# Kernel tuning notes

Measured on AMD Instinct MI355X. Metric: run time of the kernel, lower is better.

The kernel has to match this reference:

```python
import jax, jax.numpy as jnp
import numpy as np

NUM_GROUPS = 32
EPS = 1e-6


def group_norm(x, gamma, beta):
    # x: [b, c, h, w]
    b, c, h, w = x.shape
    xg = x.reshape(b, NUM_GROUPS, c // NUM_GROUPS, h, w)
    mean = xg.mean(axis=(2, 3, 4), keepdims=True)
    var = xg.var(axis=(2, 3, 4), keepdims=True)
    xn = ((xg - mean) * jax.lax.rsqrt(var + EPS)).reshape(b, c, h, w)
    return xn * gamma[None, :, None, None] + beta[None, :, None, None]


def conv1x1(x, w, bias):
    # 1x1 conv == channel-mixing matmul. x: [b,c,h,w], w: [co,ci]
    y = jnp.einsum('bchw,oc->bohw', x, w)
    return y + bias[None, :, None, None]


def setup_inputs() -> dict:
    key = jax.random.key(0)
    ks = jax.random.split(key, 10)
    B, C, H, W = 4, 512, 64, 64
    s = 1.0 / np.sqrt(C)
    inp = {
        'x': jax.random.normal(ks[0], (B, C, H, W), jnp.float32),
        'gamma': jnp.ones((C,), jnp.float32),
        'beta': jnp.zeros((C,), jnp.float32),
        'wq': jax.random.normal(ks[1], (C, C), jnp.float32) * s,
        'bq': jnp.zeros((C,), jnp.float32),
        'wk': jax.random.normal(ks[2], (C, C), jnp.float32) * s,
        'bk': jnp.zeros((C,), jnp.float32),
        'wv': jax.random.normal(ks[3], (C, C), jnp.float32) * s,
        'bv': jnp.zeros((C,), jnp.float32),
        'wo': jax.random.normal(ks[4], (C, C), jnp.float32) * s,
        'bo': jnp.zeros((C,), jnp.float32),
    }
    return inp


def reference(x, gamma, beta, wq, bq, wk, bk, wv, bv, wo, bo):
    b, c, h, w = x.shape
    h_ = group_norm(x, gamma, beta)
    q = conv1x1(h_, wq, bq).reshape(b, c, h * w)  # [b,c,n]
    k = conv1x1(h_, wk, bk).reshape(b, c, h * w)
    v = conv1x1(h_, wv, bv).reshape(b, c, h * w)
    scale = jnp.asarray(c, x.dtype) ** -0.5
    # scores: [b, n, n] = q^T k
    scores = jnp.einsum('bcn,bcm->bnm', q, k) * scale
    attn = jax.nn.softmax(scores, axis=2)
    # out: [b, c, n] = v @ attn^T  (h_[i] = sum_j attn[i,j] v[j])
    out = jnp.einsum('bnm,bcm->bcn', attn, v).reshape(b, c, h, w)
    out = conv1x1(out, wo, bo)
    return x + out
```

## Files before the change

kernel.cpp:

```cpp
#include <hip/hip_runtime.h>

typedef __bf16 bf16x8 __attribute__((ext_vector_type(8)));
typedef float f32x4 __attribute__((ext_vector_type(4)));
typedef unsigned short u16;

__device__ __forceinline__ u16 f2bf(float f) {
  unsigned int u = __builtin_bit_cast(unsigned int, f);
  u += 0x7fff + ((u >> 16) & 1);
  return (u16)(u >> 16);
}
__device__ __forceinline__ float bf2f(u16 s) {
  unsigned int u = ((unsigned int)s) << 16;
  return __builtin_bit_cast(float, u);
}
__device__ __forceinline__ void unp8(uint4 u, float* f) {
  f[0] = bf2f(u.x & 0xffff); f[1] = bf2f(u.x >> 16);
  f[2] = bf2f(u.y & 0xffff); f[3] = bf2f(u.y >> 16);
  f[4] = bf2f(u.z & 0xffff); f[5] = bf2f(u.z >> 16);
  f[6] = bf2f(u.w & 0xffff); f[7] = bf2f(u.w >> 16);
}
__device__ __forceinline__ uint4 pk8(const float* f) {
  uint4 u;
  u.x = (unsigned)f2bf(f[0]) | ((unsigned)f2bf(f[1]) << 16);
  u.y = (unsigned)f2bf(f[2]) | ((unsigned)f2bf(f[3]) << 16);
  u.z = (unsigned)f2bf(f[4]) | ((unsigned)f2bf(f[5]) << 16);
  u.w = (unsigned)f2bf(f[6]) | ((unsigned)f2bf(f[7]) << 16);
  return u;
}

__device__ __forceinline__ void gl_lds16(const u16* g, u16* l) {
  __builtin_amdgcn_global_load_lds(
      (const __attribute__((address_space(1))) void*)g,
      (__attribute__((address_space(3))) void*)l, 16, 0, 0);
}

template <int MODE>
__global__ __launch_bounds__(512, 4) void gemm_lt(
    const u16* __restrict__ A, int lda, unsigned long long sA,
    const u16* __restrict__ Bt, int ldb, unsigned long long sB,
    u16* __restrict__ Cout, int ldc, unsigned long long sC,
    int K, float alpha, int tn,
    const float* __restrict__ bias_col, const float* __restrict__ bias_col2) {
  __shared__ u16 lds[24576];
  u16* As = lds;
  u16* Bs = lds + 8192;

  const int t = threadIdx.x;
  const int lane = t & 63;
  const int w = t >> 6;
  const int bz = blockIdx.z;
  A  += (size_t)bz * sA;
  Bt += (size_t)bz * sB;

  const int nwg = gridDim.x;
  const int flat = blockIdx.x;
  const int wg = (flat & 7) * (nwg >> 3) + (flat >> 3);
  const int m0 = (wg / tn) * 128;
  const int n0 = (wg % tn) * 256;

  const int NKT = K >> 6;

  const int sr = lane >> 3;
  const int sc = ((lane & 7) ^ sr) * 8;
  const u16* gA = A  + (size_t)(m0 + w * 16 + sr) * lda + sc;
  const u16* gB = Bt + (size_t)(n0 + w * 32 + sr) * ldb + sc;
  const size_t a8 = (size_t)8 * lda, b8 = (size_t)8 * ldb;
  u16* lA = As + w * 1024;
  u16* lB = Bs + w * 2048;

  const int wr = w >> 2, wc = w & 3;
  const int fr = lane & 15, kg = lane >> 4;
  const int frx = (fr & 7) << 4;

  f32x4 acc[4][4] = {};
  bf16x8 af[4][2];
  bf16x8 bqn[2];

  for (int kt = 0; kt < NKT; ++kt) {
    if (kt) __builtin_amdgcn_s_barrier();
    {
      const size_t ko = (size_t)kt * 64;
      gl_lds16(gA + ko, lA);
      gl_lds16(gA + a8 + ko, lA + 512);
#pragma unroll
      for (int j = 0; j < 4; ++j)
        gl_lds16(gB + (size_t)j * b8 + ko, lB + j * 512);
    }
    asm volatile("s_waitcnt vmcnt(0)" ::: "memory");
    __builtin_amdgcn_s_barrier();

#pragma unroll
    for (int m = 0; m < 4; ++m) {
      const int R = wr * 64 + m * 16 + fr;
#pragma unroll
      for (int kk = 0; kk < 2; ++kk)
        af[m][kk] = *reinterpret_cast<const bf16x8*>(
            As + R * 64 + (((kk * 64 + kg * 16) ^ frx) >> 1));
    }
#pragma unroll
    for (int n = 0; n < 4; ++n) {
      const int R = wc * 64 + n * 16 + fr;
#pragma unroll
      for (int kk = 0; kk < 2; ++kk)
        bqn[kk] = *reinterpret_cast<const bf16x8*>(
            Bs + R * 64 + (((kk * 64 + kg * 16) ^ frx) >> 1));
#pragma unroll
      for (int kk = 0; kk < 2; ++kk)
#pragma unroll
        for (int m = 0; m < 4; ++m)
          acc[m][n] = __builtin_amdgcn_mfma_f32_16x16x32_bf16(
              af[m][kk], bqn[kk], acc[m][n], 0, 0, 0);
    }
  }

  u16* cs = lds;
  const size_t cbs = (size_t)bz * sC;
#pragma unroll
  for (int h = 0; h < 2; ++h) {
    __syncthreads();
    if (wr == h) {
#pragma unroll
      for (int m = 0; m < 4; ++m) {
        const int rl = m * 16 + (kg << 2);
#pragma unroll
        for (int n = 0; n < 4; ++n) {
          const int col = wc * 64 + n * 16 + fr;
          float bc = 0.0f;
          if (MODE == 0 && bias_col) {
            const int gc = n0 + col;
            bc = (bias_col2 && gc >= 512) ? bias_col2[gc - 512] : bias_col[gc & 511];
          }
#pragma unroll
          for (int r = 0; r < 4; ++r) {
            float v;
            if (MODE == 1) v = exp2f(acc[m][n][r] * alpha);
            else v = acc[m][n][r] * alpha + bc;
            cs[(rl + r) * 256 + col] = f2bf(v);
          }
        }
      }
    }
    __syncthreads();
#pragma unroll
    for (int it = 0; it < 4; ++it) {
      const int off = (it * 512 + t) * 8;
      const int row = off >> 8, col = off & 255;
      *reinterpret_cast<uint4*>(
          &Cout[cbs + (size_t)(m0 + h * 64 + row) * ldc + (n0 + col)]) =
          *reinterpret_cast<const uint4*>(&cs[off]);
    }
  }
}

template <int MODE>
__global__ __launch_bounds__(512, 2) void gemm_nt256(
    const u16* __restrict__ A, int lda, unsigned long long sA,
    const u16* __restrict__ Bt, int ldb, unsigned long long sB,
    u16* __restrict__ Cout, int ldc, unsigned long long sC,
    unsigned long long sSplit, int K, float alpha, int tn,
    float* __restrict__ psum) {
  __shared__ u16 lds[2][4][8192];

  const int t = threadIdx.x;
  const int lane = t & 63;
  const int w = t >> 6;
  const int bz = blockIdx.z;
  A  += (size_t)bz * sA + (size_t)blockIdx.y * K;
  Bt += (size_t)bz * sB + (size_t)blockIdx.y * K;
  Cout += (size_t)blockIdx.y * sSplit;

  const int nwg = gridDim.x;
  const int flat = blockIdx.x;
  const int wg = (flat & 7) * (nwg >> 3) + (flat >> 3);
  const int tt = tn << 1;
  const int p  = wg / tt;
  const int rr = wg - p * tt;
  const int m0 = (p * 2 + (rr & 1)) * 256;
  const int n0 = (rr >> 1) * 256;

  const int NKT = K >> 6;

  const int sr = lane >> 3;
  const int sc = ((lane & 7) ^ sr) * 8;
  const u16* gA = A  + (size_t)(m0 + w * 16 + sr) * lda + sc;
  const u16* gB = Bt + (size_t)(n0 + w * 16 + sr) * ldb + sc;
  const size_t a128 = (size_t)128 * lda, b128 = (size_t)128 * ldb;
  const size_t a8 = (size_t)8 * lda, b8 = (size_t)8 * ldb;
  const int lws = w * 1024;

  auto stage = [&](int slot, int region, int kt) {
    kt = kt < NKT ? kt : NKT - 1;
    u16* l = &lds[slot][region][lws];
    if (region < 2) {
      const u16* g = gA + (region ? a128 : 0) + (size_t)kt * 64;
      gl_lds16(g, l);
      gl_lds16(g + a8, l + 512);
    } else {
      const u16* g = gB + (region == 3 ? b128 : 0) + (size_t)kt * 64;
      gl_lds16(g, l);
      gl_lds16(g + b8, l + 512);
    }
  };

  const int wr = w >> 2, wc = w & 3;
  const int fr = lane & 15, kg = lane >> 4;
  const int frx = (fr & 7) << 4;

  f32x4 acc[8][4] = {};
  f32x4 sacc[8] = {};
  bf16x8 af[4][2], bq[2][2];
  union { u16 u[8]; bf16x8 v; } ou;
#pragma unroll
  for (int i = 0; i < 8; ++i) ou.u[i] = 0x3F80;
  const bf16x8 onesb = ou.v;

#define LDA_(s, qm)                                                            \
  {                                                                            \
    const u16* Ab = &lds[s][0][0];                                             \
    _Pragma("unroll") for (int m = 0; m < 4; ++m) {                            \
      const int R = wr * 128 + (qm) * 64 + m * 16 + fr;                        \
      _Pragma("unroll") for (int kk = 0; kk < 2; ++kk)                         \
          af[m][kk] = *reinterpret_cast<const bf16x8*>(                        \
              Ab + R * 64 + (((kk * 64 + kg * 16) ^ frx) >> 1));               \
    }                                                                          \
  }
#define LDB_(s, qn)                                                            \
  {                                                                            \
    const u16* Bb = &lds[s][2][0];                                             \
    _Pragma("unroll") for (int n = 0; n < 2; ++n) {                            \
      const int R = wc * 64 + (qn) * 32 + n * 16 + fr;                         \
      _Pragma("unroll") for (int kk = 0; kk < 2; ++kk)                         \
          bq[n][kk] = *reinterpret_cast<const bf16x8*>(                        \
              Bb + R * 64 + (((kk * 64 + kg * 16) ^ frx) >> 1));               \
    }                                                                          \
  }
#define PH(s, qm, qn, DOA, DOB, ss, rr_, kt, VM)                               \
  {                                                                            \
    if (DOA) LDA_(s, qm)                                                       \
    if (DOB) LDB_(s, qn)                                                       \
    stage(ss, rr_, kt);                                                        \
    __builtin_amdgcn_s_barrier();                                              \
    asm volatile("s_waitcnt lgkmcnt(0)" ::: "memory");                         \
    __builtin_amdgcn_s_setprio(1);                                             \
    _Pragma("unroll") for (int kk = 0; kk < 2; ++kk)                           \
    _Pragma("unroll") for (int m = 0; m < 4; ++m)                              \
    _Pragma("unroll") for (int n = 0; n < 2; ++n)                              \
        acc[(qm)*4 + m][(qn)*2 + n] = __builtin_amdgcn_mfma_f32_16x16x32_bf16( \
            af[m][kk], bq[n][kk], acc[(qm)*4 + m][(qn)*2 + n], 0, 0, 0);       \
    if (MODE == 2 && (DOA) && wc == 0) {                                       \
      _Pragma("unroll") for (int kk = 0; kk < 2; ++kk)                         \
      _Pragma("unroll") for (int m = 0; m < 4; ++m)                            \
          sacc[(qm)*4 + m] = __builtin_amdgcn_mfma_f32_16x16x32_bf16(          \
              af[m][kk], onesb, sacc[(qm)*4 + m], 0, 0, 0);                    \
    }                                                                          \
    __builtin_amdgcn_s_setprio(0);                                             \
    if (VM) asm volatile("s_waitcnt vmcnt(2)" ::: "memory");                   \
    __builtin_amdgcn_s_barrier();                                              \
  }

  stage(0, 0, 0); stage(0, 1, 0); stage(0, 2, 0); stage(0, 3, 0);
  stage(1, 0, 1);
  asm volatile("s_waitcnt vmcnt(2)" ::: "memory");
  __builtin_amdgcn_s_barrier();

  for (int j = 0; j < (NKT >> 1); ++j) {
    const int k1 = 2 * j + 1, k2 = 2 * j + 2, k3 = 2 * j + 3;
    PH(0, 0, 0, 1, 1, 1, 1, k1, 0)
    PH(0, 0, 1, 0, 1, 1, 2, k1, 0)
    PH(0, 1, 1, 1, 0, 1, 3, k1, 0)
    PH(0, 1, 0, 0, 1, 0, 0, k2, 1)
    PH(1, 0, 0, 1, 1, 0, 1, k2, 0)
    PH(1, 0, 1, 0, 1, 0, 2, k2, 0)
    PH(1, 1, 1, 1, 0, 0, 3, k2, 0)
    PH(1, 1, 0, 0, 1, 1, 0, k3, 1)
  }
#undef PH
#undef LDB_
#undef LDA_

  __syncthreads();
  u16* cs = &lds[0][0][0];
#pragma unroll
  for (int a = 0; a < 8; ++a) {
    const int row = wr * 128 + a * 16 + (kg << 2);
#pragma unroll
    for (int b = 0; b < 4; ++b) {
      const int col = wc * 64 + b * 16 + fr;
#pragma unroll
      for (int r = 0; r < 4; ++r)
        cs[(row + r) * 256 + col] = f2bf(acc[a][b][r] * alpha);
    }
  }
  __syncthreads();
  const size_t cbs = (size_t)bz * sC;
#pragma unroll
  for (int it = 0; it < 16; ++it) {
    const int off = (it * 512 + t) * 8;
    const int row = off >> 8, col = off & 255;
    *reinterpret_cast<uint4*>(&Cout[cbs + (size_t)(m0 + row) * ldc + (n0 + col)]) =
        *reinterpret_cast<const uint4*>(&cs[off]);
  }
  if (MODE == 2 && psum && wc == 0 && fr == 0) {
    const int Mrows = (nwg / tn) << 8;
    float* pp = psum + ((size_t)bz * gridDim.y + blockIdx.y) * Mrows + m0;
#pragma unroll
    for (int q = 0; q < 2; ++q)
#pragma unroll
      for (int m = 0; m < 4; ++m)
#pragma unroll
        for (int r = 0; r < 4; ++r)
          pp[wr * 128 + q * 64 + m * 16 + (kg << 2) + r] = sacc[q * 4 + m][r];
  }
}

template <bool OUT_F32>
__global__ __launch_bounds__(256) void gemm_nt(
    const u16* __restrict__ A, int lda, unsigned long long sA,
    const u16* __restrict__ Bt, int ldb, unsigned long long sB,
    void* __restrict__ Cout, int ldc, unsigned long long sC,
    int K, float alpha,
    const float* __restrict__ bias_row, const float* __restrict__ bias_col,
    const float* __restrict__ residual, unsigned long long sRes) {
  __shared__ u16 lds[128 * 128];
  u16* As = lds;
  u16* Bs = lds + 8192;

  const int t = threadIdx.x;
  const int bz = blockIdx.z;
  A  += (size_t)bz * sA;
  Bt += (size_t)bz * sB;
  const int m0 = blockIdx.x * 128;
  const int n0 = blockIdx.y * 128;

  const int lane = t & 63;
  const int w = t >> 6;

  const int srow = w * 32 + (lane >> 3);
  const int scol = (lane & 7) * 8;
  const u16* gA = A  + (size_t)(m0 + srow) * lda + scol;
  const u16* gB = Bt + (size_t)(n0 + srow) * ldb + scol;
  u16* lA = As + w * 2048;
  u16* lB = Bs + w * 2048;

  f32x4 acc[4][4] = {};
  const int wm = (w >> 1) * 64;
  const int wn = (w & 1) * 64;
  const int fr = lane & 15;
  const int kg = lane >> 4;

  for (int k0 = 0; k0 < K; k0 += 64) {
    __syncthreads();
#pragma unroll
    for (int i = 0; i < 4; ++i) {
      gl_lds16(gA + (size_t)(i * 8) * lda + k0, lA + i * 512);
      gl_lds16(gB + (size_t)(i * 8) * ldb + k0, lB + i * 512);
    }
    __syncthreads();

#pragma unroll
    for (int kk = 0; kk < 2; ++kk) {
      bf16x8 af[4], bfr[4];
#pragma unroll
      for (int m = 0; m < 4; ++m)
        af[m] = *reinterpret_cast<const bf16x8*>(
            &As[(wm + m * 16 + fr) * 64 + kk * 32 + kg * 8]);
#pragma unroll
      for (int n = 0; n < 4; ++n)
        bfr[n] = *reinterpret_cast<const bf16x8*>(
            &Bs[(wn + n * 16 + fr) * 64 + kk * 32 + kg * 8]);
#pragma unroll
      for (int m = 0; m < 4; ++m)
#pragma unroll
        for (int n = 0; n < 4; ++n)
          acc[m][n] = __builtin_amdgcn_mfma_f32_16x16x32_bf16(af[m], bfr[n], acc[m][n], 0, 0, 0);
    }
  }

  const size_t cbase = (size_t)bz * sC;
  const size_t rbase = (size_t)bz * sRes;
  const int rq = kg * 4;

  if (OUT_F32) {
    float* Cf = reinterpret_cast<float*>(Cout);
    float* lf = reinterpret_cast<float*>(lds);
#pragma unroll
    for (int h = 0; h < 2; ++h) {
      __syncthreads();
      if ((wm >> 6) == h) {
#pragma unroll
        for (int m = 0; m < 4; ++m)
#pragma unroll
          for (int n = 0; n < 4; ++n) {
            const float bc = bias_col ? bias_col[n0 + wn + n * 16 + fr] : 0.0f;
#pragma unroll
            for (int r = 0; r < 4; ++r)
              lf[(m * 16 + rq + r) * 128 + (wn + n * 16 + fr)] =
                  acc[m][n][r] * alpha + bc;
          }
      }
      __syncthreads();
#pragma unroll
      for (int it = 0; it < 8; ++it) {
        const int off = (it * 256 + t) * 4;
        const int row = off >> 7, col = off & 127;
        const int grow = m0 + h * 64 + row, gcol = n0 + col;
        float4 v = *reinterpret_cast<const float4*>(&lf[off]);
        if (bias_row) {
          const float br = bias_row[grow];
          v.x += br; v.y += br; v.z += br; v.w += br;
        }
        if (residual) {
          const float4 rx = *reinterpret_cast<const float4*>(
              &residual[rbase + (size_t)grow * ldc + gcol]);
          v.x += rx.x; v.y += rx.y; v.z += rx.z; v.w += rx.w;
        }
        *reinterpret_cast<float4*>(&Cf[cbase + (size_t)grow * ldc + gcol]) = v;
      }
    }
  } else {
    __syncthreads();
#pragma unroll
    for (int m = 0; m < 4; ++m) {
#pragma unroll
      for (int n = 0; n < 4; ++n) {
        const int gcol = n0 + wn + n * 16 + fr;
        const float bc = bias_col ? bias_col[gcol] : 0.0f;
#pragma unroll
        for (int r = 0; r < 4; ++r) {
          const int grow = m0 + wm + m * 16 + rq + r;
          float v = acc[m][n][r] * alpha + bc;
          if (bias_row) v += bias_row[grow];
          lds[(wm + m * 16 + rq + r) * 128 + (wn + n * 16 + fr)] = f2bf(v);
        }
      }
    }
    __syncthreads();
    u16* Cb = reinterpret_cast<u16*>(Cout);
#pragma unroll
    for (int j = 0; j < 8; ++j) {
      const int off = (j * 256 + t) * 8;
      const int row = off >> 7, col = off & 127;
      *reinterpret_cast<uint4*>(&Cb[cbase + (size_t)(m0 + row) * ldc + (n0 + col)]) =
          *reinterpret_cast<const uint4*>(&lds[off]);
    }
  }
}

__global__ __launch_bounds__(256) void groupnorm_k(
    const float* __restrict__ x, const float* __restrict__ gamma,
    const float* __restrict__ beta, u16* __restrict__ h_t, int C, int N) {
  const int g = blockIdx.x;
  const int b = blockIdx.y;
  const int t = threadIdx.x;
  const float* xb = x + ((size_t)b * C + g * 16) * N;

  float s = 0.f, q = 0.f;
  for (int c = 0; c < 16; ++c) {
    const float4* xr = reinterpret_cast<const float4*>(xb + (size_t)c * N);
    for (int j = t; j < N / 4; j += 256) {
      float4 v = xr[j];
      s += v.x + v.y + v.z + v.w;
      q += v.x * v.x + v.y * v.y + v.z * v.z + v.w * v.w;
    }
  }
#pragma unroll
  for (int o = 32; o > 0; o >>= 1) { s += __shfl_down(s, o); q += __shfl_down(q, o); }
  __shared__ float rs[4], rqs[4], stats[2];
  const int lane = t & 63, wid = t >> 6;
  if (lane == 0) { rs[wid] = s; rqs[wid] = q; }
  __syncthreads();
  if (t == 0) {
    float S = rs[0] + rs[1] + rs[2] + rs[3];
    float Q = rqs[0] + rqs[1] + rqs[2] + rqs[3];
    const float inv = 1.0f / (16.0f * (float)N);
    float mean = S * inv;
    float var = Q * inv - mean * mean;
    stats[0] = mean;
    stats[1] = rsqrtf(var + 1e-6f);
  }
  __syncthreads();
  const float mean = stats[0], rstd = stats[1];

  float gm[16], bt[16];
#pragma unroll
  for (int c = 0; c < 16; ++c) {
    gm[c] = gamma[g * 16 + c] * rstd;
    bt[c] = beta[g * 16 + c] - mean * gm[c];
  }
  u16* ho = h_t + (size_t)b * N * C + g * 16;
  for (int n = t; n < N; n += 256) {
    union { u16 us[16]; uint4 v4[2]; } pk;
#pragma unroll
    for (int c = 0; c < 16; ++c) {
      float v = xb[(size_t)c * N + n];
      pk.us[c] = f2bf(v * gm[c] + bt[c]);
    }
    uint4* dst = reinterpret_cast<uint4*>(ho + (size_t)n * C);
    dst[0] = pk.v4[0];
    dst[1] = pk.v4[1];
  }
}

__global__ __launch_bounds__(256) void wcvt4(
    const float* __restrict__ s0, const float* __restrict__ s1,
    const float* __restrict__ s2, const float* __restrict__ s3,
    u16* __restrict__ dst, int n) {
  const int i = (blockIdx.x * 256 + threadIdx.x) * 8;
  if (i >= n) return;
  const float* src = (blockIdx.y == 0) ? s0 : (blockIdx.y == 1) ? s1
                     : (blockIdx.y == 2) ? s2 : s3;
  const float4* s4 = reinterpret_cast<const float4*>(src + i);
  float4 a = s4[0], b = s4[1];
  float f[8] = {a.x, a.y, a.z, a.w, b.x, b.y, b.z, b.w};
  *reinterpret_cast<uint4*>(dst + (size_t)blockIdx.y * n + i) = pk8(f);
}

__global__ __launch_bounds__(256) void reduce_pv(const u16* __restrict__ p,
                                                 const float* __restrict__ psum,
                                                 u16* __restrict__ o, int n) {
  const int i = (blockIdx.x * 256 + threadIdx.x) * 8;
  if (i >= n) return;
  const int row = i >> 9;
  const int b = row >> 12, nn = row & 4095;
  const float il = 1.0f / (psum[(size_t)(b * 2) * 4096 + nn] +
                           psum[(size_t)(b * 2 + 1) * 4096 + nn]);
  uint4 a = *reinterpret_cast<const uint4*>(p + i);
  uint4 bb = *reinterpret_cast<const uint4*>(p + n + i);
  float fa[8], fb[8];
  unp8(a, fa); unp8(bb, fb);
#pragma unroll
  for (int j = 0; j < 8; ++j) fa[j] = (fa[j] + fb[j]) * il;
  *reinterpret_cast<uint4*>(o + i) = pk8(fa);
}

__global__ __launch_bounds__(256) void scale_o(u16* __restrict__ o,
                                               const float* __restrict__ psum,
                                               int n) {
  const int i = (blockIdx.x * 256 + threadIdx.x) * 8;
  if (i >= n) return;
  const float il = 1.0f / psum[i >> 9];
  uint4 a = *reinterpret_cast<const uint4*>(o + i);
  float fa[8];
  unp8(a, fa);
#pragma unroll
  for (int j = 0; j < 8; ++j) fa[j] *= il;
  *reinterpret_cast<uint4*>(o + i) = pk8(fa);
}

extern "C" void kernel_launch(void* const* d_in, const int* in_sizes, int n_in,
                              void* d_out, int out_size, void* d_ws, size_t ws_size,
                              hipStream_t stream) {
  const float* x     = (const float*)d_in[0];
  const float* gamma = (const float*)d_in[1];
  const float* beta  = (const float*)d_in[2];
  const float* wq    = (const float*)d_in[3];
  const float* bq    = (const float*)d_in[4];
  const float* wk    = (const float*)d_in[5];
  const float* bk    = (const float*)d_in[6];
  const float* wv    = (const float*)d_in[7];
  const float* bv    = (const float*)d_in[8];
  const float* wo    = (const float*)d_in[9];
  const float* bo    = (const float*)d_in[10];

  const int B = 4, C = 512, N = 4096;
  const size_t NC = (size_t)N * C;
  const size_t NN = (size_t)N * N;
  const size_t CC = (size_t)C * C;

  char* ws = (char*)d_ws;
  size_t off = 0;
  auto alloc = [&](size_t bytes) {
    size_t r = off;
    off = (off + bytes + 255) & ~(size_t)255;
    return r;
  };
  u16* wq_b = (u16*)(ws + alloc(CC * 2));
  u16* wk_b = (u16*)(ws + alloc(CC * 2));
  u16* wv_b = (u16*)(ws + alloc(CC * 2));
  u16* wo_b = (u16*)(ws + alloc(CC * 2));
  u16* h_t  = (u16*)(ws + alloc(B * NC * 2));
  u16* qk_t = (u16*)(ws + alloc(B * N * 1024 * 2));
  u16* v_cn = (u16*)(ws + alloc(B * NC * 2));
  u16* o_t  = (u16*)(ws + alloc(B * NC * 2));
  float* psum = (float*)(ws + alloc((size_t)B * 2 * N * 4));
  const size_t base_need = off;

  int s_batched = 0;
  u16* S;
  if (ws_size >= base_need + B * NN * 2) {
    S = (u16*)(ws + alloc(B * NN * 2));
    s_batched = 1;
  } else {
    S = (u16*)(ws + alloc(NN * 2));
  }
  u16* o_part = qk_t;

  (void)wk_b; (void)wv_b;

  wcvt4<<<dim3(CC / 2048, 4), 256, 0, stream>>>(wq, wk, wv, wo, wq_b, (int)CC);

  groupnorm_k<<<dim3(32, B), 256, 0, stream>>>(x, gamma, beta, h_t, C, N);

  gemm_lt<0><<<dim3((N / 128) * (1024 / 256), 1, B), 512, 0, stream>>>(
      h_t, C, NC, wq_b, C, 0, qk_t, 1024, (unsigned long long)N * 1024,
      C, 1.0f, 1024 / 256, bq, bk);
  dim3 gv(C / 128, N / 128, B);
  gemm_nt<false><<<gv, 256, 0, stream>>>(wv_b, C, 0, h_t, C, NC, v_cn, N, NC,
                                         C, 1.0f, bv, nullptr, nullptr, 0);

  const float c1 = 0.06376694387439652f;
  if (s_batched) {
    gemm_lt<1><<<dim3((N / 128) * (N / 256), 1, B), 512, 0, stream>>>(
        qk_t, 1024, (unsigned long long)N * 1024, qk_t + 512, 1024,
        (unsigned long long)N * 1024, S, N, NN, C, c1, N / 256,
        nullptr, nullptr);
    gemm_nt256<2><<<dim3((N / 256) * (C / 256), 2, B), 512, 0, stream>>>(
        S, N, NN, v_cn, N, NC, o_part, C, NC, (unsigned long long)B * NC,
        N / 2, 1.0f, C / 256, psum);
    reduce_pv<<<dim3((int)(B * NC / 2048)), 256, 0, stream>>>(
        o_part, psum, o_t, (int)(B * NC));
  } else {
    for (int b = 0; b < B; ++b) {
      gemm_lt<1><<<dim3((N / 128) * (N / 256), 1, 1), 512, 0, stream>>>(
          qk_t + (size_t)b * N * 1024, 1024, 0, qk_t + (size_t)b * N * 1024 + 512,
          1024, 0, S, N, 0, C, c1, N / 256, nullptr, nullptr);
      gemm_nt256<2><<<dim3((N / 256) * (C / 256), 1, 1), 512, 0, stream>>>(
          S, N, 0, v_cn + (size_t)b * NC, N, 0, o_t + (size_t)b * NC, C, 0, 0,
          N, 1.0f, C / 256, psum + (size_t)b * N);
    }
    scale_o<<<dim3((int)(B * NC / 2048)), 256, 0, stream>>>(o_t, psum, (int)(B * NC));
  }

  dim3 gf(C / 128, N / 128, B);
  gemm_nt<true><<<gf, 256, 0, stream>>>(wo_b, C, 0, o_t, C, NC, d_out, N, NC,
                                        C, 1.0f, bo, nullptr, x, NC);
}
```

Before: 302.7 us.

## Split group norm into partial-stats and apply kernels with 4x more blocks

Result: faster. 285.2 us, median of 2 (-5.8%).

```diff
diff --git a/kernel.cpp b/kernel.cpp
--- a/kernel.cpp
+++ b/kernel.cpp
@@ -125,16 +125,16 @@
 #pragma unroll
         for (int n = 0; n < 4; ++n) {
           const int col = wc * 64 + n * 16 + fr;
-          float bc = 0.0f;
+          float bcc = 0.0f;
           if (MODE == 0 && bias_col) {
             const int gc = n0 + col;
-            bc = (bias_col2 && gc >= 512) ? bias_col2[gc - 512] : bias_col[gc & 511];
+            bcc = (bias_col2 && gc >= 512) ? bias_col2[gc - 512] : bias_col[gc & 511];
           }
 #pragma unroll
           for (int r = 0; r < 4; ++r) {
-            float v;
-            if (MODE == 1) v = exp2f(acc[m][n][r] * alpha);
-            else v = acc[m][n][r] * alpha + bc;
+            float v = acc[m][n][r] * alpha;
+            if (MODE == 1) v = exp2f(v);
+            else v += bcc;
             cs[(rl + r) * 256 + col] = f2bf(v);
           }
         }
@@ -446,40 +446,44 @@
   }
 }
 
-__global__ __launch_bounds__(256) void groupnorm_k(
-    const float* __restrict__ x, const float* __restrict__ gamma,
-    const float* __restrict__ beta, u16* __restrict__ h_t, int C, int N) {
-  const int g = blockIdx.x;
-  const int b = blockIdx.y;
+__global__ __launch_bounds__(256) void gn_part(
+    const float* __restrict__ x, float2* __restrict__ part, int C, int N) {
+  const int g = blockIdx.x, b = blockIdx.y, ch = blockIdx.z;
   const int t = threadIdx.x;
-  const float* xb = x + ((size_t)b * C + g * 16) * N;
+  const float* xb = x + ((size_t)b * C + g * 16) * N + ch * (N >> 2);
 
   float s = 0.f, q = 0.f;
+#pragma unroll
   for (int c = 0; c < 16; ++c) {
-    const float4* xr = reinterpret_cast<const float4*>(xb + (size_t)c * N);
-    for (int j = t; j < N / 4; j += 256) {
-      float4 v = xr[j];
-      s += v.x + v.y + v.z + v.w;
-      q += v.x * v.x + v.y * v.y + v.z * v.z + v.w * v.w;
-    }
+    const float4 v = reinterpret_cast<const float4*>(xb + (size_t)c * N)[t];
+    s += v.x + v.y + v.z + v.w;
+    q += v.x * v.x + v.y * v.y + v.z * v.z + v.w * v.w;
   }
 #pragma unroll
   for (int o = 32; o > 0; o >>= 1) { s += __shfl_down(s, o); q += __shfl_down(q, o); }
-  __shared__ float rs[4], rqs[4], stats[2];
+  __shared__ float rs[4], rq[4];
   const int lane = t & 63, wid = t >> 6;
-  if (lane == 0) { rs[wid] = s; rqs[wid] = q; }
+  if (lane == 0) { rs[wid] = s; rq[wid] = q; }
   __syncthreads();
   if (t == 0) {
-    float S = rs[0] + rs[1] + rs[2] + rs[3];
-    float Q = rqs[0] + rqs[1] + rqs[2] + rqs[3];
-    const float inv = 1.0f / (16.0f * (float)N);
-    float mean = S * inv;
-    float var = Q * inv - mean * mean;
-    stats[0] = mean;
-    stats[1] = rsqrtf(var + 1e-6f);
-  }
-  __syncthreads();
-  const float mean = stats[0], rstd = stats[1];
+    part[(((size_t)b * 32 + g) << 2) + ch] =
+        make_float2(rs[0] + rs[1] + rs[2] + rs[3], rq[0] + rq[1] + rq[2] + rq[3]);
+  }
+}
+
+__global__ __launch_bounds__(256) void gn_apply(
+    const float* __restrict__ x, const float* __restrict__ gamma,
+    const float* __restrict__ beta, const float2* __restrict__ part,
+    u16* __restrict__ h_t, int C, int N) {
+  const int g = blockIdx.x, b = blockIdx.y, ch = blockIdx.z;
+  const int t = threadIdx.x;
+  const float2* pp = &part[(((size_t)b * 32 + g) << 2)];
+  const float2 p0 = pp[0], p1 = pp[1], p2 = pp[2], p3 = pp[3];
+  const float S = p0.x + p1.x + p2.x + p3.x;
+  const float Q = p0.y + p1.y + p2.y + p3.y;
+  const float inv = 1.0f / (16.0f * (float)N);
+  const float mean = S * inv;
+  const float rstd = rsqrtf(Q * inv - mean * mean + 1e-6f);
 
   float gm[16], bt[16];
 #pragma unroll
@@ -487,8 +491,10 @@
     gm[c] = gamma[g * 16 + c] * rstd;
     bt[c] = beta[g * 16 + c] - mean * gm[c];
   }
+  const float* xb = x + ((size_t)b * C + g * 16) * N;
   u16* ho = h_t + (size_t)b * N * C + g * 16;
-  for (int n = t; n < N; n += 256) {
+  const int n0 = ch * (N >> 2);
+  for (int n = n0 + t; n < n0 + (N >> 2); n += 256) {
     union { u16 us[16]; uint4 v4[2]; } pk;
 #pragma unroll
     for (int c = 0; c < 16; ++c) {
@@ -583,6 +589,7 @@
   u16* v_cn = (u16*)(ws + alloc(B * NC * 2));
   u16* o_t  = (u16*)(ws + alloc(B * NC * 2));
   float* psum = (float*)(ws + alloc((size_t)B * 2 * N * 4));
+  float2* gnp = (float2*)(ws + alloc((size_t)B * 32 * 4 * 8));
   const size_t base_need = off;
 
   int s_batched = 0;
@@ -595,11 +602,12 @@
   }
   u16* o_part = qk_t;
 
-  (void)wk_b; (void)wv_b;
+  (void)wk_b;
 
   wcvt4<<<dim3(CC / 2048, 4), 256, 0, stream>>>(wq, wk, wv, wo, wq_b, (int)CC);
 
-  groupnorm_k<<<dim3(32, B), 256, 0, stream>>>(x, gamma, beta, h_t, C, N);
+  gn_part<<<dim3(32, B, 4), 256, 0, stream>>>(x, gnp, C, N);
+  gn_apply<<<dim3(32, B, 4), 256, 0, stream>>>(x, gamma, beta, gnp, h_t, C, N);
 
   gemm_lt<0><<<dim3((N / 128) * (1024 / 256), 1, B), 512, 0, stream>>>(
       h_t, C, NC, wq_b, C, 0, qk_t, 1024, (unsigned long long)N * 1024,
```
